# Performance work log

Measured on AMD Instinct MI355X. Metric: run time of the kernel, lower is better.

Reference implementation:

```python
import jax, jax.numpy as jnp
import numpy as np

N_NODES = 100000
N_EDGES = 1600000
IN_DIM = 128
HID = 64
CONV2_OUT = 8
GLOBAL_DIM = 24
OUT_DIM = 1
NUM_GRAPHS = 64
NEG_SLOPE = 0.01


def setup_inputs() -> dict:
    key = jax.random.key(0)
    ks = jax.random.split(key, 12)
    x = jax.random.normal(ks[0], (N_NODES, IN_DIM), dtype=jnp.float32)
    edge_index = jax.random.randint(ks[1], (2, N_EDGES), 0, N_NODES, dtype=jnp.int32)
    batch = jnp.sort(jax.random.randint(ks[2], (N_NODES,), 0, NUM_GRAPHS, dtype=jnp.int32))
    global_features = jax.random.normal(ks[3], (NUM_GRAPHS, GLOBAL_DIM), dtype=jnp.float32)
    # GCNConv weights (glorot-ish scale) and Linear weights
    W1 = jax.random.normal(ks[4], (IN_DIM, HID), dtype=jnp.float32) / np.sqrt(IN_DIM)
    b1 = jnp.zeros((HID,), dtype=jnp.float32)
    W2 = jax.random.normal(ks[5], (HID, CONV2_OUT), dtype=jnp.float32) / np.sqrt(HID)
    b2 = jnp.zeros((CONV2_OUT,), dtype=jnp.float32)
    fcW1 = jax.random.normal(ks[6], (GLOBAL_DIM + CONV2_OUT, 16), dtype=jnp.float32) / np.sqrt(GLOBAL_DIM + CONV2_OUT)
    fcb1 = jnp.zeros((16,), dtype=jnp.float32)
    fcW2 = jax.random.normal(ks[7], (16, OUT_DIM), dtype=jnp.float32) / np.sqrt(16)
    fcb2 = jnp.zeros((OUT_DIM,), dtype=jnp.float32)
    return {"x": x, "edge_index": edge_index, "batch": batch,
            "global_features": global_features,
            "W1": W1, "b1": b1, "W2": W2, "b2": b2,
            "fcW1": fcW1, "fcb1": fcb1, "fcW2": fcW2, "fcb2": fcb2}


def gcn_conv(x, src, dst, W, b):
    """PyG GCNConv: add self-loops, sym-normalize, aggregate x@W from src->dst."""
    n = x.shape[0]
    h = x @ W  # [N, F_out]
    loop = jnp.arange(n, dtype=src.dtype)
    src2 = jnp.concatenate([src, loop])
    dst2 = jnp.concatenate([dst, loop])
    deg = jax.ops.segment_sum(jnp.ones_like(dst2, dtype=h.dtype), dst2, num_segments=n)
    dinv = jnp.where(deg > 0, jax.lax.rsqrt(deg), 0.0)
    norm = dinv[src2] * dinv[dst2]  # [E+N]
    msg = h[src2] * norm[:, None]   # edge gather (dominant traffic)
    out = jax.ops.segment_sum(msg, dst2, num_segments=n)
    return out + b


def reference(x, edge_index, batch, global_features, W1, b1, W2, b2, fcW1, fcb1, fcW2, fcb2):
    src, dst = edge_index[0], edge_index[1]
    h = jax.nn.leaky_relu(gcn_conv(x, src, dst, W1, b1), NEG_SLOPE)
    h = jax.nn.leaky_relu(gcn_conv(h, src, dst, W2, b2), NEG_SLOPE)
    # global mean pool over graphs
    sums = jax.ops.segment_sum(h, batch, num_segments=NUM_GRAPHS)
    cnts = jax.ops.segment_sum(jnp.ones((h.shape[0],), h.dtype), batch, num_segments=NUM_GRAPHS)
    pool = sums / jnp.maximum(cnts, 1.0)[:, None]
    z = jnp.concatenate([pool, global_features], axis=1)
    z = jax.nn.leaky_relu(z @ fcW1 + fcb1, NEG_SLOPE)
    z = jax.nn.leaky_relu(z @ fcW2 + fcb2, NEG_SLOPE)
    return z
```

## Files before the change

kernel.cpp:

```cpp
#include <hip/hip_runtime.h>

constexpr int N_NODES = 100000;
constexpr int N_EDGES = 1600000;
constexpr int IN_DIM  = 128;
constexpr int HID     = 64;
constexpr int C2      = 8;
constexpr int GDIM    = 24;
constexpr int NG      = 64;
constexpr float SLOPE = 0.01f;
constexpr int NB_SCAN = (N_NODES + 255) / 256;

__device__ __forceinline__ float lrelu(float v) { return v > 0.f ? v : SLOPE * v; }

__global__ void k_rank(const int* __restrict__ dst, int* __restrict__ deg,
                       int* __restrict__ rnk) {
    int e = blockIdx.x * 256 + threadIdx.x;
    if (e < N_EDGES) rnk[e] = atomicAdd(&deg[dst[e]], 1);
}

__global__ void k_dinv(const int* __restrict__ deg, float* __restrict__ dinv,
                       float* __restrict__ gacc) {
    int i = blockIdx.x * 256 + threadIdx.x;
    if (i < N_NODES) dinv[i] = rsqrtf((float)(deg[i] + 1));
    if (blockIdx.x == 0)
        for (int j = threadIdx.x; j < NG * C2 + NG; j += 256) gacc[j] = 0.f;
}

__global__ void k_scan1(const int* __restrict__ deg, int* __restrict__ rowptr,
                        int* __restrict__ bsum) {
    __shared__ int s[256];
    int tid = threadIdx.x;
    int i = blockIdx.x * 256 + tid;
    int v = (i < N_NODES) ? deg[i] : 0;
    s[tid] = v;
    __syncthreads();
    for (int off = 1; off < 256; off <<= 1) {
        int t = (tid >= off) ? s[tid - off] : 0;
        __syncthreads();
        s[tid] += t;
        __syncthreads();
    }
    if (i < N_NODES) rowptr[i] = s[tid] - v;
    if (tid == 255) bsum[blockIdx.x] = s[255];
}

__global__ void k_scan2(const int* __restrict__ bsum, int* __restrict__ bsumx) {
    __shared__ int s[512];
    int tid = threadIdx.x;
    int v = (tid < NB_SCAN) ? bsum[tid] : 0;
    s[tid] = v;
    __syncthreads();
    for (int off = 1; off < 512; off <<= 1) {
        int t = (tid >= off) ? s[tid - off] : 0;
        __syncthreads();
        s[tid] += t;
        __syncthreads();
    }
    if (tid < NB_SCAN) bsumx[tid] = s[tid] - v;
}

__global__ void k_scan3(int* __restrict__ rowptr, const int* __restrict__ bsumx) {
    int i = blockIdx.x * 256 + threadIdx.x;
    if (i < N_NODES) rowptr[i] += bsumx[blockIdx.x];
}

__global__ void k_place(const int* __restrict__ src, const int* __restrict__ dst,
                        const int* __restrict__ rnk, const int* __restrict__ rowptr,
                        int* __restrict__ eidx) {
    int e = blockIdx.x * 256 + threadIdx.x;
    if (e < N_EDGES) eidx[rowptr[dst[e]] + rnk[e]] = src[e];
}

__global__ __launch_bounds__(256) void k_gemm1(const float* __restrict__ x,
                                               const float* __restrict__ W1,
                                               const float* __restrict__ dinv,
                                               float* __restrict__ hs1) {
    __shared__ float sW[IN_DIM * HID];
    __shared__ float sX[32][IN_DIM];
    int node0 = blockIdx.x * 32;
    for (int t = threadIdx.x; t < IN_DIM * HID / 4; t += 256)
        ((float4*)sW)[t] = ((const float4*)W1)[t];
    for (int t = threadIdx.x; t < 32 * IN_DIM / 4; t += 256) {
        int r = t >> 5, c4 = t & 31;
        ((float4*)&sX[r][0])[c4] = ((const float4*)(x + (size_t)(node0 + r) * IN_DIM))[c4];
    }
    __syncthreads();
    int col = threadIdx.x & 63;
    int nb  = (threadIdx.x >> 6) * 8;
    float acc[8] = {0.f, 0.f, 0.f, 0.f, 0.f, 0.f, 0.f, 0.f};
#pragma unroll 4
    for (int k = 0; k < IN_DIM; ++k) {
        float wv = sW[k * HID + col];
#pragma unroll
        for (int j = 0; j < 8; ++j) acc[j] += sX[nb + j][k] * wv;
    }
#pragma unroll
    for (int j = 0; j < 8; ++j) {
        int n = node0 + nb + j;
        hs1[(size_t)n * HID + col] = acc[j] * dinv[n];
    }
}

__global__ __launch_bounds__(256) void k_agg1(const int* __restrict__ rowptr,
                                              const int* __restrict__ deg,
                                              const int* __restrict__ eidx,
                                              const float* __restrict__ hs1,
                                              const float* __restrict__ dinv,
                                              const float* __restrict__ b1,
                                              const float* __restrict__ W2,
                                              float* __restrict__ hs2) {
    __shared__ float sW2t[C2 * HID];
    for (int i = threadIdx.x; i < HID * C2; i += 256) {
        int k = i >> 3, j = i & 7;
        sW2t[j * HID + k] = W2[i];
    }
    __syncthreads();
    int node = blockIdx.x * 4 + (threadIdx.x >> 6);
    int lane = threadIdx.x & 63;
    int q    = lane & 15;
    int slot = lane >> 4;
    int start = rowptr[node];
    int cnt   = deg[node];
    float4 acc = make_float4(0.f, 0.f, 0.f, 0.f);
    for (int k = slot; k < cnt; k += 4) {
        int s = eidx[start + k];
        float4 v = ((const float4*)(hs1 + (size_t)s * HID))[q];
        acc.x += v.x; acc.y += v.y; acc.z += v.z; acc.w += v.w;
    }
    acc.x += __shfl_xor(acc.x, 16); acc.y += __shfl_xor(acc.y, 16);
    acc.z += __shfl_xor(acc.z, 16); acc.w += __shfl_xor(acc.w, 16);
    acc.x += __shfl_xor(acc.x, 32); acc.y += __shfl_xor(acc.y, 32);
    acc.z += __shfl_xor(acc.z, 32); acc.w += __shfl_xor(acc.w, 32);
    float4 h  = ((const float4*)(hs1 + (size_t)node * HID))[q];
    float  di = dinv[node];
    float4 bb = ((const float4*)b1)[q];
    float4 y;
    y.x = lrelu(di * (acc.x + h.x) + bb.x);
    y.y = lrelu(di * (acc.y + h.y) + bb.y);
    y.z = lrelu(di * (acc.z + h.z) + bb.z);
    y.w = lrelu(di * (acc.w + h.w) + bb.w);
    int j0 = slot * 2;
    const float* w0 = sW2t + j0 * HID + 4 * q;
    const float* w1 = w0 + HID;
    float p0 = y.x * w0[0] + y.y * w0[1] + y.z * w0[2] + y.w * w0[3];
    float p1 = y.x * w1[0] + y.y * w1[1] + y.z * w1[2] + y.w * w1[3];
#pragma unroll
    for (int m = 1; m < 16; m <<= 1) {
        p0 += __shfl_xor(p0, m);
        p1 += __shfl_xor(p1, m);
    }
    if (q == 0) {
        float2 r; r.x = p0 * di; r.y = p1 * di;
        ((float2*)(hs2 + (size_t)node * C2))[slot] = r;
    }
}

__global__ __launch_bounds__(256) void k_agg2(const int* __restrict__ rowptr,
                                              const int* __restrict__ deg,
                                              const int* __restrict__ eidx,
                                              const float* __restrict__ hs2,
                                              const float* __restrict__ dinv,
                                              const float* __restrict__ b2,
                                              float* __restrict__ y2) {
    int node = blockIdx.x * 4 + (threadIdx.x >> 6);
    int lane = threadIdx.x & 63;
    int q    = lane & 1;
    int slot = lane >> 1;
    int start = rowptr[node];
    int cnt   = deg[node];
    float4 acc = make_float4(0.f, 0.f, 0.f, 0.f);
    for (int k = slot; k < cnt; k += 32) {
        int s = eidx[start + k];
        float4 v = ((const float4*)(hs2 + (size_t)s * C2))[q];
        acc.x += v.x; acc.y += v.y; acc.z += v.z; acc.w += v.w;
    }
    for (int m = 2; m < 64; m <<= 1) {
        acc.x += __shfl_xor(acc.x, m); acc.y += __shfl_xor(acc.y, m);
        acc.z += __shfl_xor(acc.z, m); acc.w += __shfl_xor(acc.w, m);
    }
    if (slot == 0) {
        float4 h = ((const float4*)(hs2 + (size_t)node * C2))[q];
        float di = dinv[node];
        const float* bb = b2 + q * 4;
        float4 r;
        r.x = lrelu(di * (acc.x + h.x) + bb[0]);
        r.y = lrelu(di * (acc.y + h.y) + bb[1]);
        r.z = lrelu(di * (acc.z + h.z) + bb[2]);
        r.w = lrelu(di * (acc.w + h.w) + bb[3]);
        ((float4*)(y2 + (size_t)node * C2))[q] = r;
    }
}

__global__ __launch_bounds__(256) void k_pool(const float* __restrict__ y2,
                                              const int* __restrict__ batch,
                                              float* __restrict__ gsum,
                                              float* __restrict__ gcnt) {
    __shared__ float ssum[NG * C2];
    __shared__ float scnt[NG];
    for (int i = threadIdx.x; i < NG * C2; i += 256) ssum[i] = 0.f;
    for (int i = threadIdx.x; i < NG; i += 256) scnt[i] = 0.f;
    __syncthreads();
    int node = blockIdx.x * 32 + (threadIdx.x >> 3);
    int col  = threadIdx.x & 7;
    if (node < N_NODES) {
        int g = batch[node];
        float v = y2[(size_t)node * C2 + col];
        atomicAdd(&ssum[g * C2 + col], v);
        if (col == 0) atomicAdd(&scnt[g], 1.f);
    }
    __syncthreads();
    for (int i = threadIdx.x; i < NG * C2; i += 256)
        if (ssum[i] != 0.f) atomicAdd(&gsum[i], ssum[i]);
    for (int i = threadIdx.x; i < NG; i += 256)
        if (scnt[i] != 0.f) atomicAdd(&gcnt[i], scnt[i]);
}

__global__ void k_mlp(const float* __restrict__ gsum, const float* __restrict__ gcnt,
                      const float* __restrict__ gfeat,
                      const float* __restrict__ fcW1, const float* __restrict__ fcb1,
                      const float* __restrict__ fcW2, const float* __restrict__ fcb2,
                      float* __restrict__ out) {
    int g = threadIdx.x;
    if (g >= NG) return;
    float z[C2 + GDIM];
    float cnt = fmaxf(gcnt[g], 1.f);
    for (int c = 0; c < C2; ++c) z[c] = gsum[g * C2 + c] / cnt;
    for (int c = 0; c < GDIM; ++c) z[C2 + c] = gfeat[g * GDIM + c];
    float h16[16];
    for (int j = 0; j < 16; ++j) {
        float acc = fcb1[j];
        for (int c = 0; c < C2 + GDIM; ++c) acc += z[c] * fcW1[c * 16 + j];
        h16[j] = lrelu(acc);
    }
    float acc = fcb2[0];
    for (int j = 0; j < 16; ++j) acc += h16[j] * fcW2[j];
    out[g] = lrelu(acc);
}

extern "C" void kernel_launch(void* const* d_in, const int* in_sizes, int n_in,
                              void* d_out, int out_size, void* d_ws, size_t ws_size,
                              hipStream_t stream) {
    const float* x     = (const float*)d_in[0];
    const int*   ei    = (const int*)d_in[1];
    const int*   batch = (const int*)d_in[2];
    const float* gfeat = (const float*)d_in[3];
    const float* W1    = (const float*)d_in[4];
    const float* b1    = (const float*)d_in[5];
    const float* W2    = (const float*)d_in[6];
    const float* b2    = (const float*)d_in[7];
    const float* fcW1  = (const float*)d_in[8];
    const float* fcb1  = (const float*)d_in[9];
    const float* fcW2  = (const float*)d_in[10];
    const float* fcb2  = (const float*)d_in[11];
    const int* src = ei;
    const int* dst = ei + N_EDGES;

    char* ws = (char*)d_ws;
    size_t off = 0;
    auto alloc = [&](size_t bytes) -> void* {
        void* p = ws + off;
        off = (off + bytes + 255) & ~(size_t)255;
        return p;
    };
    int*   deg    = (int*)  alloc((size_t)N_NODES * 4);
    float* dinv   = (float*)alloc((size_t)N_NODES * 4);
    int*   rowptr = (int*)  alloc((size_t)N_NODES * 4);
    int*   bsum   = (int*)  alloc(512 * 4);
    int*   bsumx  = (int*)  alloc(512 * 4);
    int*   rnk    = (int*)  alloc((size_t)N_EDGES * 4);
    int*   eidx   = (int*)  alloc((size_t)N_EDGES * 4);
    float* hs1    = (float*)alloc((size_t)N_NODES * HID * 4);
    float* hs2    = (float*)alloc((size_t)N_NODES * C2 * 4);
    float* y2     = (float*)alloc((size_t)N_NODES * C2 * 4);
    float* gacc   = (float*)alloc((size_t)(NG * C2 + NG) * 4);
    float* gsum   = gacc;
    float* gcnt   = gacc + NG * C2;

    hipMemsetAsync(deg, 0, (size_t)N_NODES * 4, stream);

    k_rank <<<(N_EDGES + 255) / 256, 256, 0, stream>>>(dst, deg, rnk);
    k_dinv <<<NB_SCAN, 256, 0, stream>>>(deg, dinv, gacc);
    k_scan1<<<NB_SCAN, 256, 0, stream>>>(deg, rowptr, bsum);
    k_scan2<<<1, 512, 0, stream>>>(bsum, bsumx);
    k_scan3<<<NB_SCAN, 256, 0, stream>>>(rowptr, bsumx);
    k_place<<<(N_EDGES + 255) / 256, 256, 0, stream>>>(src, dst, rnk, rowptr, eidx);

    k_gemm1<<<N_NODES / 32, 256, 0, stream>>>(x, W1, dinv, hs1);
    k_agg1 <<<N_NODES / 4, 256, 0, stream>>>(rowptr, deg, eidx, hs1, dinv, b1, W2, hs2);
    k_agg2 <<<N_NODES / 4, 256, 0, stream>>>(rowptr, deg, eidx, hs2, dinv, b2, y2);
    k_pool <<<(N_NODES + 31) / 32, 256, 0, stream>>>(y2, batch, gsum, gcnt);
    k_mlp  <<<1, 64, 0, stream>>>(gsum, gcnt, gfeat, fcW1, fcb1, fcW2, fcb2, (float*)d_out);
}
```

Baseline: 289.0 us.

## Store hs1 in bf16, fuse pooling into agg2, and drop scan/dinv kernels

Stores the layer-1 transformed features as bf16, halving the bytes read by the dominant edge gather in agg1. The dinv computation moves into scan1, accumulator zeroing moves into scan2, and the scan3 pass is removed by adding the block offset wherever rowptr is read. The pooling reduction is fused into agg2 so y2 is never written, and the gemm1 inner loop is vectorised with float4 shared reads. The cost is lost precision in the hidden features and more shared-memory atomics inside agg2.

```diff
diff --git a/kernel.cpp b/kernel.cpp
--- a/kernel.cpp
+++ b/kernel.cpp
@@ -12,26 +12,30 @@
 
 __device__ __forceinline__ float lrelu(float v) { return v > 0.f ? v : SLOPE * v; }
 
+__device__ __forceinline__ float bf2f(unsigned short u) {
+    union { unsigned int i; float f; } c;
+    c.i = ((unsigned int)u) << 16;
+    return c.f;
+}
+__device__ __forceinline__ unsigned short f2bf(float f) {
+    unsigned int i = __float_as_uint(f);
+    unsigned int r = (i + 0x7fffu + ((i >> 16) & 1u)) >> 16;
+    return (unsigned short)r;
+}
+
 __global__ void k_rank(const int* __restrict__ dst, int* __restrict__ deg,
                        int* __restrict__ rnk) {
     int e = blockIdx.x * 256 + threadIdx.x;
     if (e < N_EDGES) rnk[e] = atomicAdd(&deg[dst[e]], 1);
 }
 
-__global__ void k_dinv(const int* __restrict__ deg, float* __restrict__ dinv,
-                       float* __restrict__ gacc) {
-    int i = blockIdx.x * 256 + threadIdx.x;
-    if (i < N_NODES) dinv[i] = rsqrtf((float)(deg[i] + 1));
-    if (blockIdx.x == 0)
-        for (int j = threadIdx.x; j < NG * C2 + NG; j += 256) gacc[j] = 0.f;
-}
-
 __global__ void k_scan1(const int* __restrict__ deg, int* __restrict__ rowptr,
-                        int* __restrict__ bsum) {
+                        int* __restrict__ bsum, float* __restrict__ dinv) {
     __shared__ int s[256];
     int tid = threadIdx.x;
     int i = blockIdx.x * 256 + tid;
     int v = (i < N_NODES) ? deg[i] : 0;
+    if (i < N_NODES) dinv[i] = rsqrtf((float)(v + 1));
     s[tid] = v;
     __syncthreads();
     for (int off = 1; off < 256; off <<= 1) {
@@ -44,9 +48,11 @@
     if (tid == 255) bsum[blockIdx.x] = s[255];
 }
 
-__global__ void k_scan2(const int* __restrict__ bsum, int* __restrict__ bsumx) {
+__global__ void k_scan2(const int* __restrict__ bsum, int* __restrict__ bsumx,
+                        float* __restrict__ gacc) {
     __shared__ int s[512];
     int tid = threadIdx.x;
+    for (int j = tid; j < NG * C2 + NG; j += 512) gacc[j] = 0.f;
     int v = (tid < NB_SCAN) ? bsum[tid] : 0;
     s[tid] = v;
     __syncthreads();
@@ -59,22 +65,20 @@
     if (tid < NB_SCAN) bsumx[tid] = s[tid] - v;
 }
 
-__global__ void k_scan3(int* __restrict__ rowptr, const int* __restrict__ bsumx) {
-    int i = blockIdx.x * 256 + threadIdx.x;
-    if (i < N_NODES) rowptr[i] += bsumx[blockIdx.x];
-}
-
 __global__ void k_place(const int* __restrict__ src, const int* __restrict__ dst,
                         const int* __restrict__ rnk, const int* __restrict__ rowptr,
-                        int* __restrict__ eidx) {
+                        const int* __restrict__ bsumx, int* __restrict__ eidx) {
     int e = blockIdx.x * 256 + threadIdx.x;
-    if (e < N_EDGES) eidx[rowptr[dst[e]] + rnk[e]] = src[e];
+    if (e < N_EDGES) {
+        int d = dst[e];
+        eidx[rowptr[d] + bsumx[d >> 8] + rnk[e]] = src[e];
+    }
 }
 
 __global__ __launch_bounds__(256) void k_gemm1(const float* __restrict__ x,
                                                const float* __restrict__ W1,
                                                const float* __restrict__ dinv,
-                                               float* __restrict__ hs1) {
+                                               unsigned short* __restrict__ hs1) {
     __shared__ float sW[IN_DIM * HID];
     __shared__ float sX[32][IN_DIM];
     int node0 = blockIdx.x * 32;
@@ -88,57 +92,64 @@
     int col = threadIdx.x & 63;
     int nb  = (threadIdx.x >> 6) * 8;
     float acc[8] = {0.f, 0.f, 0.f, 0.f, 0.f, 0.f, 0.f, 0.f};
-#pragma unroll 4
-    for (int k = 0; k < IN_DIM; ++k) {
-        float wv = sW[k * HID + col];
+    for (int k4 = 0; k4 < IN_DIM; k4 += 4) {
+        float w0 = sW[(k4 + 0) * HID + col];
+        float w1 = sW[(k4 + 1) * HID + col];
+        float w2 = sW[(k4 + 2) * HID + col];
+        float w3 = sW[(k4 + 3) * HID + col];
 #pragma unroll
-        for (int j = 0; j < 8; ++j) acc[j] += sX[nb + j][k] * wv;
+        for (int j = 0; j < 8; ++j) {
+            float4 xv = *((const float4*)&sX[nb + j][k4]);
+            acc[j] += xv.x * w0 + xv.y * w1 + xv.z * w2 + xv.w * w3;
+        }
     }
 #pragma unroll
     for (int j = 0; j < 8; ++j) {
         int n = node0 + nb + j;
-        hs1[(size_t)n * HID + col] = acc[j] * dinv[n];
+        hs1[(size_t)n * HID + col] = f2bf(acc[j] * dinv[n]);
     }
 }
 
 __global__ __launch_bounds__(256) void k_agg1(const int* __restrict__ rowptr,
+                                              const int* __restrict__ bsumx,
                                               const int* __restrict__ deg,
                                               const int* __restrict__ eidx,
-                                              const float* __restrict__ hs1,
+                                              const unsigned short* __restrict__ hs1,
                                               const float* __restrict__ dinv,
                                               const float* __restrict__ b1,
                                               const float* __restrict__ W2,
                                               float* __restrict__ hs2) {
     __shared__ float sW2t[C2 * HID];
-    for (int i = threadIdx.x; i < HID * C2; i += 256) {
-        int k = i >> 3, j = i & 7;
-        sW2t[j * HID + k] = W2[i];
+    for (int i = threadIdx.x; i < C2 * HID; i += 256) {
+        int j = i >> 6, k = i & 63;
+        sW2t[i] = W2[k * C2 + j];
     }
     __syncthreads();
     int node = blockIdx.x * 4 + (threadIdx.x >> 6);
     int lane = threadIdx.x & 63;
     int q    = lane & 15;
     int slot = lane >> 4;
-    int start = rowptr[node];
+    int start = rowptr[node] + bsumx[node >> 8];
     int cnt   = deg[node];
     float4 acc = make_float4(0.f, 0.f, 0.f, 0.f);
     for (int k = slot; k < cnt; k += 4) {
         int s = eidx[start + k];
-        float4 v = ((const float4*)(hs1 + (size_t)s * HID))[q];
-        acc.x += v.x; acc.y += v.y; acc.z += v.z; acc.w += v.w;
+        ushort4 v = ((const ushort4*)(hs1 + (size_t)s * HID))[q];
+        acc.x += bf2f(v.x); acc.y += bf2f(v.y);
+        acc.z += bf2f(v.z); acc.w += bf2f(v.w);
     }
     acc.x += __shfl_xor(acc.x, 16); acc.y += __shfl_xor(acc.y, 16);
     acc.z += __shfl_xor(acc.z, 16); acc.w += __shfl_xor(acc.w, 16);
     acc.x += __shfl_xor(acc.x, 32); acc.y += __shfl_xor(acc.y, 32);
     acc.z += __shfl_xor(acc.z, 32); acc.w += __shfl_xor(acc.w, 32);
-    float4 h  = ((const float4*)(hs1 + (size_t)node * HID))[q];
+    ushort4 hv = ((const ushort4*)(hs1 + (size_t)node * HID))[q];
     float  di = dinv[node];
     float4 bb = ((const float4*)b1)[q];
     float4 y;
-    y.x = lrelu(di * (acc.x + h.x) + bb.x);
-    y.y = lrelu(di * (acc.y + h.y) + bb.y);
-    y.z = lrelu(di * (acc.z + h.z) + bb.z);
-    y.w = lrelu(di * (acc.w + h.w) + bb.w);
+    y.x = lrelu(di * (acc.x + bf2f(hv.x)) + bb.x);
+    y.y = lrelu(di * (acc.y + bf2f(hv.y)) + bb.y);
+    y.z = lrelu(di * (acc.z + bf2f(hv.z)) + bb.z);
+    y.w = lrelu(di * (acc.w + bf2f(hv.w)) + bb.w);
     int j0 = slot * 2;
     const float* w0 = sW2t + j0 * HID + 4 * q;
     const float* w1 = w0 + HID;
@@ -156,42 +167,12 @@
 }
 
 __global__ __launch_bounds__(256) void k_agg2(const int* __restrict__ rowptr,
+                                              const int* __restrict__ bsumx,
                                               const int* __restrict__ deg,
                                               const int* __restrict__ eidx,
                                               const float* __restrict__ hs2,
                                               const float* __restrict__ dinv,
                                               const float* __restrict__ b2,
-                                              float* __restrict__ y2) {
-    int node = blockIdx.x * 4 + (threadIdx.x >> 6);
-    int lane = threadIdx.x & 63;
-    int q    = lane & 1;
-    int slot = lane >> 1;
-    int start = rowptr[node];
-    int cnt   = deg[node];
-    float4 acc = make_float4(0.f, 0.f, 0.f, 0.f);
-    for (int k = slot; k < cnt; k += 32) {
-        int s = eidx[start + k];
-        float4 v = ((const float4*)(hs2 + (size_t)s * C2))[q];
-        acc.x += v.x; acc.y += v.y; acc.z += v.z; acc.w += v.w;
-    }
-    for (int m = 2; m < 64; m <<= 1) {
-        acc.x += __shfl_xor(acc.x, m); acc.y += __shfl_xor(acc.y, m);
-        acc.z += __shfl_xor(acc.z, m); acc.w += __shfl_xor(acc.w, m);
-    }
-    if (slot == 0) {
-        float4 h = ((const float4*)(hs2 + (size_t)node * C2))[q];
-        float di = dinv[node];
-        const float* bb = b2 + q * 4;
-        float4 r;
-        r.x = lrelu(di * (acc.x + h.x) + bb[0]);
-        r.y = lrelu(di * (acc.y + h.y) + bb[1]);
-        r.z = lrelu(di * (acc.z + h.z) + bb[2]);
-        r.w = lrelu(di * (acc.w + h.w) + bb[3]);
-        ((float4*)(y2 + (size_t)node * C2))[q] = r;
-    }
-}
-
-__global__ __launch_bounds__(256) void k_pool(const float* __restrict__ y2,
                                               const int* __restrict__ batch,
                                               float* __restrict__ gsum,
                                               float* __restrict__ gcnt) {
@@ -200,13 +181,33 @@
     for (int i = threadIdx.x; i < NG * C2; i += 256) ssum[i] = 0.f;
     for (int i = threadIdx.x; i < NG; i += 256) scnt[i] = 0.f;
     __syncthreads();
-    int node = blockIdx.x * 32 + (threadIdx.x >> 3);
-    int col  = threadIdx.x & 7;
-    if (node < N_NODES) {
+    int node = blockIdx.x * 4 + (threadIdx.x >> 6);
+    int lane = threadIdx.x & 63;
+    int q    = lane & 1;
+    int slot = lane >> 1;
+    int start = rowptr[node] + bsumx[node >> 8];
+    int cnt   = deg[node];
+    float4 acc = make_float4(0.f, 0.f, 0.f, 0.f);
+    for (int k = slot; k < cnt; k += 32) {
+        int s = eidx[start + k];
+        float4 v = ((const float4*)(hs2 + (size_t)s * C2))[q];
+        acc.x += v.x; acc.y += v.y; acc.z += v.z; acc.w += v.w;
+    }
+    for (int m = 2; m < 64; m <<= 1) {
+        acc.x += __shfl_xor(acc.x, m); acc.y += __shfl_xor(acc.y, m);
+        acc.z += __shfl_xor(acc.z, m); acc.w += __shfl_xor(acc.w, m);
+    }
+    if (slot == 0) {
+        float4 h = ((const float4*)(hs2 + (size_t)node * C2))[q];
+        float di = dinv[node];
+        const float* bb = b2 + q * 4;
         int g = batch[node];
-        float v = y2[(size_t)node * C2 + col];
-        atomicAdd(&ssum[g * C2 + col], v);
-        if (col == 0) atomicAdd(&scnt[g], 1.f);
+        float* sb = ssum + g * C2 + q * 4;
+        atomicAdd(sb + 0, lrelu(di * (acc.x + h.x) + bb[0]));
+        atomicAdd(sb + 1, lrelu(di * (acc.y + h.y) + bb[1]));
+        atomicAdd(sb + 2, lrelu(di * (acc.z + h.z) + bb[2]));
+        atomicAdd(sb + 3, lrelu(di * (acc.w + h.w) + bb[3]));
+        if (q == 0) atomicAdd(&scnt[g], 1.f);
     }
     __syncthreads();
     for (int i = threadIdx.x; i < NG * C2; i += 256)
@@ -269,9 +270,8 @@
     int*   bsumx  = (int*)  alloc(512 * 4);
     int*   rnk    = (int*)  alloc((size_t)N_EDGES * 4);
     int*   eidx   = (int*)  alloc((size_t)N_EDGES * 4);
-    float* hs1    = (float*)alloc((size_t)N_NODES * HID * 4);
+    unsigned short* hs1 = (unsigned short*)alloc((size_t)N_NODES * HID * 2);
     float* hs2    = (float*)alloc((size_t)N_NODES * C2 * 4);
-    float* y2     = (float*)alloc((size_t)N_NODES * C2 * 4);
     float* gacc   = (float*)alloc((size_t)(NG * C2 + NG) * 4);
     float* gsum   = gacc;
     float* gcnt   = gacc + NG * C2;
@@ -279,15 +279,12 @@
     hipMemsetAsync(deg, 0, (size_t)N_NODES * 4, stream);
 
     k_rank <<<(N_EDGES + 255) / 256, 256, 0, stream>>>(dst, deg, rnk);
-    k_dinv <<<NB_SCAN, 256, 0, stream>>>(deg, dinv, gacc);
-    k_scan1<<<NB_SCAN, 256, 0, stream>>>(deg, rowptr, bsum);
-    k_scan2<<<1, 512, 0, stream>>>(bsum, bsumx);
-    k_scan3<<<NB_SCAN, 256, 0, stream>>>(rowptr, bsumx);
-    k_place<<<(N_EDGES + 255) / 256, 256, 0, stream>>>(src, dst, rnk, rowptr, eidx);
+    k_scan1<<<NB_SCAN, 256, 0, stream>>>(deg, rowptr, bsum, dinv);
+    k_scan2<<<1, 512, 0, stream>>>(bsum, bsumx, gacc);
+    k_place<<<(N_EDGES + 255) / 256, 256, 0, stream>>>(src, dst, rnk, rowptr, bsumx, eidx);
 
     k_gemm1<<<N_NODES / 32, 256, 0, stream>>>(x, W1, dinv, hs1);
-    k_agg1 <<<N_NODES / 4, 256, 0, stream>>>(rowptr, deg, eidx, hs1, dinv, b1, W2, hs2);
-    k_agg2 <<<N_NODES / 4, 256, 0, stream>>>(rowptr, deg, eidx, hs2, dinv, b2, y2);
-    k_pool <<<(N_NODES + 31) / 32, 256, 0, stream>>>(y2, batch, gsum, gcnt);
+    k_agg1 <<<N_NODES / 4, 256, 0, stream>>>(rowptr, bsumx, deg, eidx, hs1, dinv, b1, W2, hs2);
+    k_agg2 <<<N_NODES / 4, 256, 0, stream>>>(rowptr, bsumx, deg, eidx, hs2, dinv, b2, batch, gsum, gcnt);
     k_mlp  <<<1, 64, 0, stream>>>(gsum, gcnt, gfeat, fcW1, fcb1, fcW2, fcb2, (float*)d_out);
 }
```

Result: slower. 490.0 us (+69.5%).
